# Performance work log

Hardware: AMD Instinct MI355X
Metric: run time of the kernel (lower is better)

Reference implementation:

```python
import jax, jax.numpy as jnp
import numpy as np

BN_EPS = 1e-3  # Keras BatchNormalization default epsilon


def setup_inputs() -> dict:
    key = jax.random.key(0)
    ks = jax.random.split(key, 5)
    B, H, W, C = 8, 64, 64, 256
    c = C // 4  # downsize_factor = 4
    OC = 256
    return {
        "x": jax.random.normal(ks[0], (B, H, W, C), dtype=jnp.float32),
        "Wk": jax.random.normal(ks[1], (C, c), dtype=jnp.float32) * 0.05,
        "Wq": jax.random.normal(ks[2], (C, c), dtype=jnp.float32) * 0.05,
        "Wv": jax.random.normal(ks[3], (C, c), dtype=jnp.float32) * 0.05,
        "Wo": jax.random.normal(ks[4], (c, OC), dtype=jnp.float32) * 0.05,
        "gamma": jnp.ones((OC,), dtype=jnp.float32),
        "beta": jnp.zeros((OC,), dtype=jnp.float32),
        "moving_mean": jnp.zeros((OC,), dtype=jnp.float32),
        "moving_var": jnp.ones((OC,), dtype=jnp.float32),
    }


def reference(x, Wk, Wq, Wv, Wo, gamma, beta, moving_mean, moving_var):
    B, H, W, C = x.shape
    c = Wk.shape[1]
    # 1x1 convs (no bias) == per-position matmuls; flatten spatial to N = H*W
    xf = x.reshape(B, H * W, C)
    k = xf @ Wk  # [B, N, c]
    q = xf @ Wq  # [B, N, c]
    v = xf @ Wv  # [B, N, c]
    # Keras Dot(axes=2)([key, query]): scores[b,i,j] = sum_c k[b,i,c]*q[b,j,c]  (unscaled)
    scores = jnp.einsum('bic,bjc->bij', k, q)  # [B, N, N]
    attn = jax.nn.softmax(scores, axis=-1)
    # Dot(axes=(2,1))([attn, value])
    out = jnp.einsum('bij,bjc->bic', attn, v)  # [B, N, c]
    out = out.reshape(B, H, W, c)
    # output 1x1 conv
    out = jnp.einsum('bhwc,co->bhwo', out, Wo)
    # BatchNorm (inference, moving statistics)
    out = gamma * (out - moving_mean) * jax.lax.rsqrt(moving_var + BN_EPS) + beta
    return out
```

## Files before the change

### kernel.cpp

```cpp
#include <hip/hip_runtime.h>
#include <hip/hip_bf16.h>

typedef __bf16 bf16_8 __attribute__((ext_vector_type(8)));
typedef _Float16 f16x8 __attribute__((ext_vector_type(8)));
typedef float f32x4 __attribute__((ext_vector_type(4)));
typedef float f32x16 __attribute__((ext_vector_type(16)));

#define MFMA_BF(A, B, C)    __builtin_amdgcn_mfma_f32_16x16x32_bf16(A, B, C, 0, 0, 0)
#define MFMA_F16(A, B, C)   __builtin_amdgcn_mfma_f32_16x16x32_f16(A, B, C, 0, 0, 0)
#define MFMA32_F16(A, B, C) __builtin_amdgcn_mfma_f32_32x32x16_f16(A, B, C, 0, 0, 0)
#define MFMA32_BF(A, B, C)  __builtin_amdgcn_mfma_f32_32x32x16_bf16(A, B, C, 0, 0, 0)

#define BATCH 8
#define NPOS 4096
#define CIN 256
#define CMID 64
#define OC 256
#define NROWS (BATCH * NPOS)
#define NSPLIT 4
#define LOG2E 1.44269504088896f

__device__ inline void swaplane32(unsigned& a, unsigned& b) {
    asm volatile("v_permlane32_swap_b32 %0, %1" : "+v"(a), "+v"(b));
}

#if __has_builtin(__builtin_amdgcn_exp2f)
__device__ inline float fexp2(float x) { return __builtin_amdgcn_exp2f(x); }
#else
__device__ inline float fexp2(float x) {
    float r;
    asm("v_exp_f32 %0, %1\n\ts_nop 1" : "=v"(r) : "v"(x));
    return r;
}
#endif

__global__ __launch_bounds__(256) void proj_kernel(
    const float* __restrict__ x,
    const float* __restrict__ Wk, const float* __restrict__ Wq,
    const float* __restrict__ Wv,
    _Float16* __restrict__ k_ws, _Float16* __restrict__ q_ws,
    __bf16* __restrict__ vT_ws)
{
    const int m = blockIdx.y;
    const int r0 = blockIdx.x * 64;
    const float* W = (m == 0) ? Wk : (m == 1) ? Wq : Wv;
    const float wscale = (m == 0) ? LOG2E : 1.0f;

    __shared__ _Float16 wt[64][266];

    for (int idx = threadIdx.x; idx < 64 * 256; idx += 256) {
        int col = idx & 63, k = idx >> 6;
        wt[col][k] = (_Float16)(W[k * 64 + col] * wscale);
    }

    const int lane = threadIdx.x & 63;
    const int wv = threadIdx.x >> 6;
    const int kbase = ((lane >> 4) & 3) * 8;
    const int arow = r0 + wv * 16 + (lane & 15);
    const float* xrow = x + (size_t)arow * CIN;

    f16x8 a[8];
    #pragma unroll
    for (int kk = 0; kk < 8; ++kk) {
        const float4* xp = (const float4*)(xrow + kk * 32 + kbase);
        float4 x0 = xp[0], x1 = xp[1];
        float xs[8] = {x0.x, x0.y, x0.z, x0.w, x1.x, x1.y, x1.z, x1.w};
        #pragma unroll
        for (int e = 0; e < 8; ++e) a[kk][e] = (_Float16)xs[e];
    }
    __syncthreads();

    f32x4 acc[4] = {f32x4{0,0,0,0}, f32x4{0,0,0,0}, f32x4{0,0,0,0}, f32x4{0,0,0,0}};
    #pragma unroll
    for (int kk = 0; kk < 8; ++kk) {
        #pragma unroll
        for (int nt = 0; nt < 4; ++nt) {
            f16x8 b = *(const f16x8*)&wt[(lane & 15) + 16 * nt][kk * 32 + kbase];
            acc[nt] = MFMA_F16(a[kk], b, acc[nt]);
        }
    }

    const int rloc = wv * 16 + ((lane >> 4) & 3) * 4;
    if (m < 2) {
        __syncthreads();
        _Float16* rp = &wt[0][0];
        #pragma unroll
        for (int nt = 0; nt < 4; ++nt)
            #pragma unroll
            for (int r = 0; r < 4; ++r)
                rp[(rloc + r) * 72 + (lane & 15) + 16 * nt] = (_Float16)acc[nt][r];
        __syncthreads();
        _Float16* dst = (m == 0) ? k_ws : q_ws;
        const int row = threadIdx.x >> 3, c0 = (threadIdx.x & 7) * 8;
        #pragma unroll
        for (int h = 0; h < 2; ++h) {
            uint4 v = *(const uint4*)&rp[(row + 32 * h) * 72 + c0];
            *(uint4*)(dst + (size_t)(r0 + row + 32 * h) * CMID + c0) = v;
        }
    } else {
        const int rrow = r0 + rloc;
        const int b = rrow >> 12;
        const int n = rrow & (NPOS - 1);
        #pragma unroll
        for (int nt = 0; nt < 4; ++nt) {
            int cv = (lane & 15) + 16 * nt;
            union { __bf16 h[4]; uint2 u; } pk;
            #pragma unroll
            for (int r = 0; r < 4; ++r) pk.h[r] = (__bf16)acc[nt][r];
            *(uint2*)(vT_ws + ((size_t)b * CMID + cv) * NPOS + n) = pk.u;
        }
    }
}

__global__ __launch_bounds__(512, 4) void flash_kernel(
    const _Float16* __restrict__ k_ws,
    const _Float16* __restrict__ q_ws,
    const __bf16* __restrict__ vT_ws,
    __bf16* __restrict__ po,
    float* __restrict__ pden)
{
    const int b = blockIdx.y;
    const int i0 = blockIdx.x * 256;
    const int sblk = blockIdx.z;
    const int jbase = sblk * (NPOS / NSPLIT);
    const int lane = threadIdx.x & 63;
    const int wv = threadIdx.x >> 6;
    const int l31 = lane & 31;
    const int g = lane >> 5;

    __shared__ _Float16 qt[2][64][72];
    __shared__ __bf16 vt[2][64][72];

    f16x8 kf[4];
    {
        const _Float16* kp =
            k_ws + ((size_t)(b * NPOS + i0 + wv * 32 + l31)) * CMID + g * 8;
        #pragma unroll
        for (int c = 0; c < 4; ++c) kf[c] = *(const f16x8*)(kp + c * 16);
    }

    bf16_8 vone;
    #pragma unroll
    for (int e = 0; e < 8; ++e) vone[e] = (__bf16)1.0f;

    f32x16 o0 = {0,0,0,0,0,0,0,0,0,0,0,0,0,0,0,0};
    f32x16 o1 = {0,0,0,0,0,0,0,0,0,0,0,0,0,0,0,0};
    f32x16 o_den = {0,0,0,0,0,0,0,0,0,0,0,0,0,0,0,0};

    const int r = threadIdx.x >> 3, c0 = (threadIdx.x & 7) * 8;
    uint4 nq, nv;

    {
        nq = *(const uint4*)(q_ws + ((size_t)(b * NPOS + jbase + r)) * CMID + c0);
        nv = *(const uint4*)(vT_ws + ((size_t)b * CMID + r) * NPOS + jbase + c0);
        *(uint4*)&qt[0][r][c0] = nq;
        *(uint4*)&vt[0][r][c0] = nv;
    }
    __syncthreads();

    const int NT = (NPOS / NSPLIT) / 64;
    for (int t = 0; t < NT; ++t) {
        const int cur = t & 1;
        if (t + 1 < NT) {
            int j1 = jbase + (t + 1) * 64;
            nq = *(const uint4*)(q_ws + ((size_t)(b * NPOS + j1 + r)) * CMID + c0);
            nv = *(const uint4*)(vT_ws + ((size_t)b * CMID + r) * NPOS + j1 + c0);
        }

        #pragma unroll
        for (int jj = 0; jj < 2; ++jj) {
            f16x8 aq[4];
            #pragma unroll
            for (int c = 0; c < 4; ++c)
                aq[c] = *(const f16x8*)&qt[cur][jj * 32 + l31][c * 16 + g * 8];
            bf16_8 bv00 = *(const bf16_8*)&vt[cur][l31][jj * 32 + g * 8];
            bf16_8 bv01 = *(const bf16_8*)&vt[cur][l31][jj * 32 + 16 + g * 8];
            bf16_8 bv10 = *(const bf16_8*)&vt[cur][32 + l31][jj * 32 + g * 8];
            bf16_8 bv11 = *(const bf16_8*)&vt[cur][32 + l31][jj * 32 + 16 + g * 8];

            __builtin_amdgcn_s_setprio(1);
            f32x16 s = {0,0,0,0,0,0,0,0,0,0,0,0,0,0,0,0};
            s = MFMA32_F16(aq[0], kf[0], s);
            s = MFMA32_F16(aq[1], kf[1], s);
            s = MFMA32_F16(aq[2], kf[2], s);
            s = MFMA32_F16(aq[3], kf[3], s);
            __builtin_amdgcn_s_setprio(0);

            unsigned pk[8];
            #pragma unroll
            for (int m = 0; m < 8; ++m) {
                float p0 = fexp2(s[2 * m]);
                float p1 = fexp2(s[2 * m + 1]);
                union { __bf16 h[2]; unsigned u; } w;
                w.h[0] = (__bf16)p0; w.h[1] = (__bf16)p1;
                pk[m] = w.u;
            }
            swaplane32(pk[0], pk[2]); swaplane32(pk[1], pk[3]);
            swaplane32(pk[4], pk[6]); swaplane32(pk[5], pk[7]);
            union { unsigned u[4]; bf16_8 v; } pa0, pa1;
            pa0.u[0] = pk[0]; pa0.u[1] = pk[1]; pa0.u[2] = pk[2]; pa0.u[3] = pk[3];
            pa1.u[0] = pk[4]; pa1.u[1] = pk[5]; pa1.u[2] = pk[6]; pa1.u[3] = pk[7];

            __builtin_amdgcn_s_setprio(1);
            o0 = MFMA32_BF(pa0.v, bv00, o0);
            o0 = MFMA32_BF(pa1.v, bv01, o0);
            o1 = MFMA32_BF(pa0.v, bv10, o1);
            o1 = MFMA32_BF(pa1.v, bv11, o1);
            o_den = MFMA32_BF(pa0.v, vone, o_den);
            o_den = MFMA32_BF(pa1.v, vone, o_den);
            __builtin_amdgcn_s_setprio(0);
        }

        if (t + 1 < NT) {
            const int nb = cur ^ 1;
            *(uint4*)&qt[nb][r][c0] = nq;
            *(uint4*)&vt[nb][r][c0] = nv;
        }
        __syncthreads();
    }

    const size_t rowb = (size_t)b * NPOS + i0 + wv * 32;

    if (l31 == 0) {
        #pragma unroll
        for (int reg = 0; reg < 16; ++reg) {
            int il = (reg & 3) + 8 * (reg >> 2) + 4 * g;
            pden[(size_t)sblk * NROWS + rowb + il] = o_den[reg];
        }
    }

    #pragma unroll
    for (int reg = 0; reg < 16; ++reg) {
        int il = (reg & 3) + 8 * (reg >> 2) + 4 * g;
        size_t base = ((size_t)sblk * NROWS + rowb + il) * CMID + l31;
        po[base]      = (__bf16)o0[reg];
        po[base + 32] = (__bf16)o1[reg];
    }
}

__global__ __launch_bounds__(256) void out_kernel(
    const __bf16* __restrict__ po,
    const float* __restrict__ pden,
    const float* __restrict__ Wo,
    const float* __restrict__ gamma, const float* __restrict__ beta,
    const float* __restrict__ mmean, const float* __restrict__ mvar,
    float* __restrict__ out)
{
    const int r0 = blockIdx.x * 16;
    const int t = threadIdx.x;
    const int lane = t & 63;
    const int wv = t >> 6;
    const int n0 = wv * 64;

    __shared__ __bf16 at[16][72];
    __shared__ float dinv[16];
    __shared__ float ot[16][260];

    bf16_8 wb[4][2];
    #pragma unroll
    for (int nt = 0; nt < 4; ++nt) {
        int col = n0 + nt * 16 + (lane & 15);
        #pragma unroll
        for (int ch = 0; ch < 2; ++ch)
            #pragma unroll
            for (int e = 0; e < 8; ++e)
                wb[nt][ch][e] = (__bf16)Wo[(ch * 32 + (lane >> 4) * 8 + e) * OC + col];
    }

    if (t < 16) {
        float d = 0.f;
        #pragma unroll
        for (int s = 0; s < NSPLIT; ++s) d += pden[(size_t)s * NROWS + r0 + t];
        dinv[t] = 1.0f / d;
    }
    __syncthreads();

    {
        int rr = t >> 4, c4 = (t & 15) * 4;
        float s0 = 0.f, s1 = 0.f, s2 = 0.f, s3 = 0.f;
        #pragma unroll
        for (int s = 0; s < NSPLIT; ++s) {
            union { uint2 u; __bf16 h[4]; } q;
            q.u = *(const uint2*)&po[((size_t)s * NROWS + r0 + rr) * CMID + c4];
            s0 += (float)q.h[0]; s1 += (float)q.h[1];
            s2 += (float)q.h[2]; s3 += (float)q.h[3];
        }
        float di = dinv[rr];
        union { __bf16 h[4]; uint2 u; } o;
        o.h[0] = (__bf16)(s0 * di); o.h[1] = (__bf16)(s1 * di);
        o.h[2] = (__bf16)(s2 * di); o.h[3] = (__bf16)(s3 * di);
        *(uint2*)&at[rr][c4] = o.u;
    }
    __syncthreads();

    bf16_8 a0 = *(const bf16_8*)&at[lane & 15][(lane >> 4) * 8];
    bf16_8 a1 = *(const bf16_8*)&at[lane & 15][32 + (lane >> 4) * 8];

    #pragma unroll
    for (int nt = 0; nt < 4; ++nt) {
        int col = n0 + nt * 16 + (lane & 15);
        f32x4 acc = {0.f, 0.f, 0.f, 0.f};
        acc = MFMA_BF(a0, wb[nt][0], acc);
        acc = MFMA_BF(a1, wb[nt][1], acc);
        float sc = gamma[col] * rsqrtf(mvar[col] + 1e-3f);
        float sh = beta[col] - mmean[col] * sc;
        int rl = (lane >> 4) * 4;
        #pragma unroll
        for (int rr = 0; rr < 4; ++rr)
            ot[rl + rr][col] = acc[rr] * sc + sh;
    }
    __syncthreads();

    {
        const int sr = t >> 6;
        const int sc4 = (t & 63) * 4;
        #pragma unroll
        for (int p = 0; p < 4; ++p) {
            int row = p * 4 + sr;
            float4 v = *(const float4*)&ot[row][sc4];
            *(float4*)&out[(size_t)(r0 + row) * OC + sc4] = v;
        }
    }
}

extern "C" void kernel_launch(void* const* d_in, const int* in_sizes, int n_in,
                              void* d_out, int out_size, void* d_ws, size_t ws_size,
                              hipStream_t stream) {
    const float* x     = (const float*)d_in[0];
    const float* Wk    = (const float*)d_in[1];
    const float* Wq    = (const float*)d_in[2];
    const float* Wv    = (const float*)d_in[3];
    const float* Wo    = (const float*)d_in[4];
    const float* gamma = (const float*)d_in[5];
    const float* beta  = (const float*)d_in[6];
    const float* mmean = (const float*)d_in[7];
    const float* mvar  = (const float*)d_in[8];
    float* out = (float*)d_out;

    char* ob = (char*)d_out;
    const size_t MB4 = (size_t)NROWS * CMID * 2;
    _Float16* k_ws = (_Float16*)ob;
    _Float16* q_ws = (_Float16*)(ob + MB4);
    __bf16*   vT   = (__bf16*)(ob + 2 * MB4);

    __bf16* po   = (__bf16*)d_ws;
    float*  pden = (float*)((char*)d_ws + (size_t)NSPLIT * MB4);

    proj_kernel<<<dim3(512, 3), 256, 0, stream>>>(x, Wk, Wq, Wv, k_ws, q_ws, vT);
    flash_kernel<<<dim3(16, 8, NSPLIT), 512, 0, stream>>>(k_ws, q_ws, vT, po, pden);
    out_kernel<<<2048, 256, 0, stream>>>(po, pden, Wo, gamma, beta, mmean, mvar, out);
}
```

Before: 91.83 us.

## Precompute fp16 weights once, fuse K/Q/V projections, compute softmax denominator with VALU

A small kernel now transposes and converts the three projection weights to fp16 a single time, and the projection kernel computes K, Q and V in one block that reads x once, instead of three separate grid rows that each reload x and rebuild an LDS weight copy. In the flash kernel the denominator is summed with scalar adds plus a lane shuffle instead of two extra MFMAs against a ones vector, and the s_setprio hints are removed. This cuts redundant x traffic and MFMA work, in exchange for an extra kernel launch, weight B-operands read from global/cache rather than LDS, and VALU adds on the exp path.

```diff
diff --git a/kernel.cpp b/kernel.cpp
--- a/kernel.cpp
+++ b/kernel.cpp
@@ -34,24 +34,33 @@
 }
 #endif
 
+__global__ __launch_bounds__(256) void wprep_kernel(
+    const float* __restrict__ Wk, const float* __restrict__ Wq,
+    const float* __restrict__ Wv, _Float16* __restrict__ WT)
+{
+    int idx = (blockIdx.x * 256 + threadIdx.x) * 4;
+    int m = idx >> 14;
+    int rem = idx & 16383;
+    int col = rem >> 8;
+    int k0 = rem & 255;
+    const float* W = (m == 0) ? Wk : (m == 1) ? Wq : Wv;
+    float sc = (m == 0) ? LOG2E : 1.0f;
+    union { _Float16 h[4]; uint2 u; } o;
+    #pragma unroll
+    for (int r = 0; r < 4; ++r)
+        o.h[r] = (_Float16)(W[(k0 + r) * CMID + col] * sc);
+    *(uint2*)(WT + idx) = o.u;
+}
+
 __global__ __launch_bounds__(256) void proj_kernel(
     const float* __restrict__ x,
-    const float* __restrict__ Wk, const float* __restrict__ Wq,
-    const float* __restrict__ Wv,
+    const _Float16* __restrict__ WT,
     _Float16* __restrict__ k_ws, _Float16* __restrict__ q_ws,
     __bf16* __restrict__ vT_ws)
 {
-    const int m = blockIdx.y;
     const int r0 = blockIdx.x * 64;
-    const float* W = (m == 0) ? Wk : (m == 1) ? Wq : Wv;
-    const float wscale = (m == 0) ? LOG2E : 1.0f;
-
-    __shared__ _Float16 wt[64][266];
-
-    for (int idx = threadIdx.x; idx < 64 * 256; idx += 256) {
-        int col = idx & 63, k = idx >> 6;
-        wt[col][k] = (_Float16)(W[k * 64 + col] * wscale);
-    }
+
+    __shared__ _Float16 rp[2][64][72];
 
     const int lane = threadIdx.x & 63;
     const int wv = threadIdx.x >> 6;
@@ -68,47 +77,51 @@
         #pragma unroll
         for (int e = 0; e < 8; ++e) a[kk][e] = (_Float16)xs[e];
     }
-    __syncthreads();
-
-    f32x4 acc[4] = {f32x4{0,0,0,0}, f32x4{0,0,0,0}, f32x4{0,0,0,0}, f32x4{0,0,0,0}};
-    #pragma unroll
-    for (int kk = 0; kk < 8; ++kk) {
-        #pragma unroll
-        for (int nt = 0; nt < 4; ++nt) {
-            f16x8 b = *(const f16x8*)&wt[(lane & 15) + 16 * nt][kk * 32 + kbase];
-            acc[nt] = MFMA_F16(a[kk], b, acc[nt]);
-        }
-    }
 
     const int rloc = wv * 16 + ((lane >> 4) & 3) * 4;
-    if (m < 2) {
-        __syncthreads();
-        _Float16* rp = &wt[0][0];
-        #pragma unroll
-        for (int nt = 0; nt < 4; ++nt)
-            #pragma unroll
-            for (int r = 0; r < 4; ++r)
-                rp[(rloc + r) * 72 + (lane & 15) + 16 * nt] = (_Float16)acc[nt][r];
-        __syncthreads();
-        _Float16* dst = (m == 0) ? k_ws : q_ws;
-        const int row = threadIdx.x >> 3, c0 = (threadIdx.x & 7) * 8;
-        #pragma unroll
-        for (int h = 0; h < 2; ++h) {
-            uint4 v = *(const uint4*)&rp[(row + 32 * h) * 72 + c0];
-            *(uint4*)(dst + (size_t)(r0 + row + 32 * h) * CMID + c0) = v;
-        }
-    } else {
-        const int rrow = r0 + rloc;
-        const int b = rrow >> 12;
-        const int n = rrow & (NPOS - 1);
-        #pragma unroll
-        for (int nt = 0; nt < 4; ++nt) {
-            int cv = (lane & 15) + 16 * nt;
-            union { __bf16 h[4]; uint2 u; } pk;
-            #pragma unroll
-            for (int r = 0; r < 4; ++r) pk.h[r] = (__bf16)acc[nt][r];
-            *(uint2*)(vT_ws + ((size_t)b * CMID + cv) * NPOS + n) = pk.u;
-        }
+
+    #pragma unroll
+    for (int m = 0; m < 3; ++m) {
+        const _Float16* Wm = WT + m * (CMID * CIN);
+        f32x4 acc[4] = {f32x4{0,0,0,0}, f32x4{0,0,0,0}, f32x4{0,0,0,0}, f32x4{0,0,0,0}};
+        #pragma unroll
+        for (int kk = 0; kk < 8; ++kk) {
+            #pragma unroll
+            for (int nt = 0; nt < 4; ++nt) {
+                f16x8 b = *(const f16x8*)&Wm[((lane & 15) + 16 * nt) * CIN + kk * 32 + kbase];
+                acc[nt] = MFMA_F16(a[kk], b, acc[nt]);
+            }
+        }
+
+        if (m < 2) {
+            #pragma unroll
+            for (int nt = 0; nt < 4; ++nt)
+                #pragma unroll
+                for (int r = 0; r < 4; ++r)
+                    rp[m][rloc + r][(lane & 15) + 16 * nt] = (_Float16)acc[nt][r];
+        } else {
+            const int rrow = r0 + rloc;
+            const int b = rrow >> 12;
+            const int n = rrow & (NPOS - 1);
+            #pragma unroll
+            for (int nt = 0; nt < 4; ++nt) {
+                int cv = (lane & 15) + 16 * nt;
+                union { __bf16 h[4]; uint2 u; } pk;
+                #pragma unroll
+                for (int r = 0; r < 4; ++r) pk.h[r] = (__bf16)acc[nt][r];
+                *(uint2*)(vT_ws + ((size_t)b * CMID + cv) * NPOS + n) = pk.u;
+            }
+        }
+    }
+
+    __syncthreads();
+    const int row = threadIdx.x >> 3, c0 = (threadIdx.x & 7) * 8;
+    #pragma unroll
+    for (int h = 0; h < 2; ++h) {
+        uint4 vk = *(const uint4*)&rp[0][row + 32 * h][c0];
+        *(uint4*)(k_ws + (size_t)(r0 + row + 32 * h) * CMID + c0) = vk;
+        uint4 vq = *(const uint4*)&rp[1][row + 32 * h][c0];
+        *(uint4*)(q_ws + (size_t)(r0 + row + 32 * h) * CMID + c0) = vq;
     }
 }
 
@@ -139,13 +152,9 @@
         for (int c = 0; c < 4; ++c) kf[c] = *(const f16x8*)(kp + c * 16);
     }
 
-    bf16_8 vone;
-    #pragma unroll
-    for (int e = 0; e < 8; ++e) vone[e] = (__bf16)1.0f;
-
     f32x16 o0 = {0,0,0,0,0,0,0,0,0,0,0,0,0,0,0,0};
     f32x16 o1 = {0,0,0,0,0,0,0,0,0,0,0,0,0,0,0,0};
-    f32x16 o_den = {0,0,0,0,0,0,0,0,0,0,0,0,0,0,0,0};
+    float den = 0.f;
 
     const int r = threadIdx.x >> 3, c0 = (threadIdx.x & 7) * 8;
     uint4 nq, nv;
@@ -178,19 +187,18 @@
             bf16_8 bv10 = *(const bf16_8*)&vt[cur][32 + l31][jj * 32 + g * 8];
             bf16_8 bv11 = *(const bf16_8*)&vt[cur][32 + l31][jj * 32 + 16 + g * 8];
 
-            __builtin_amdgcn_s_setprio(1);
             f32x16 s = {0,0,0,0,0,0,0,0,0,0,0,0,0,0,0,0};
             s = MFMA32_F16(aq[0], kf[0], s);
             s = MFMA32_F16(aq[1], kf[1], s);
             s = MFMA32_F16(aq[2], kf[2], s);
             s = MFMA32_F16(aq[3], kf[3], s);
-            __builtin_amdgcn_s_setprio(0);
 
             unsigned pk[8];
             #pragma unroll
             for (int m = 0; m < 8; ++m) {
                 float p0 = fexp2(s[2 * m]);
                 float p1 = fexp2(s[2 * m + 1]);
+                den += p0 + p1;
                 union { __bf16 h[2]; unsigned u; } w;
                 w.h[0] = (__bf16)p0; w.h[1] = (__bf16)p1;
                 pk[m] = w.u;
@@ -201,14 +209,10 @@
             pa0.u[0] = pk[0]; pa0.u[1] = pk[1]; pa0.u[2] = pk[2]; pa0.u[3] = pk[3];
             pa1.u[0] = pk[4]; pa1.u[1] = pk[5]; pa1.u[2] = pk[6]; pa1.u[3] = pk[7];
 
-            __builtin_amdgcn_s_setprio(1);
             o0 = MFMA32_BF(pa0.v, bv00, o0);
             o0 = MFMA32_BF(pa1.v, bv01, o0);
             o1 = MFMA32_BF(pa0.v, bv10, o1);
             o1 = MFMA32_BF(pa1.v, bv11, o1);
-            o_den = MFMA32_BF(pa0.v, vone, o_den);
-            o_den = MFMA32_BF(pa1.v, vone, o_den);
-            __builtin_amdgcn_s_setprio(0);
         }
 
         if (t + 1 < NT) {
@@ -219,15 +223,11 @@
         __syncthreads();
     }
 
+    den += __shfl_xor(den, 32);
+
     const size_t rowb = (size_t)b * NPOS + i0 + wv * 32;
-
-    if (l31 == 0) {
-        #pragma unroll
-        for (int reg = 0; reg < 16; ++reg) {
-            int il = (reg & 3) + 8 * (reg >> 2) + 4 * g;
-            pden[(size_t)sblk * NROWS + rowb + il] = o_den[reg];
-        }
-    }
+    if (lane < 32)
+        pden[(size_t)sblk * NROWS + rowb + lane] = den;
 
     #pragma unroll
     for (int reg = 0; reg < 16; ++reg) {
@@ -343,10 +343,12 @@
     _Float16* q_ws = (_Float16*)(ob + MB4);
     __bf16*   vT   = (__bf16*)(ob + 2 * MB4);
 
-    __bf16* po   = (__bf16*)d_ws;
-    float*  pden = (float*)((char*)d_ws + (size_t)NSPLIT * MB4);
-
-    proj_kernel<<<dim3(512, 3), 256, 0, stream>>>(x, Wk, Wq, Wv, k_ws, q_ws, vT);
+    __bf16*    po   = (__bf16*)d_ws;
+    float*     pden = (float*)((char*)d_ws + (size_t)NSPLIT * MB4);
+    _Float16*  WT   = (_Float16*)((char*)d_ws + (size_t)NSPLIT * MB4 + (size_t)NSPLIT * NROWS * 4);
+
+    wprep_kernel<<<48, 256, 0, stream>>>(Wk, Wq, Wv, WT);
+    proj_kernel<<<512, 256, 0, stream>>>(x, WT, k_ws, q_ws, vT);
     flash_kernel<<<dim3(16, 8, NSPLIT), 512, 0, stream>>>(k_ws, q_ws, vT, po, pden);
     out_kernel<<<2048, 256, 0, stream>>>(po, pden, Wo, gamma, beta, mmean, mvar, out);
 }
```

Result: slower. 99.51 us (+8.4%).
